# Optimization experiments

Hardware: AMD Instinct MI355X
Metric: run time of the kernel (lower is better)

The kernel has to match this reference:

```python
import jax, jax.numpy as jnp
import numpy as np

N_WIRES = 5
TOTAL = 2 * N_WIRES          # query branch simulates 2*n_wires qubits
DIM = 1 << TOTAL             # 1024
ENC = 1 << N_WIRES           # 32 = token encoder output dim


def setup_inputs() -> dict:
    key = jax.random.key(0)
    ks = jax.random.split(key, 6)
    B, T, C = 4, 32, 512
    x = jax.random.normal(ks[0], (B, T, C), jnp.float32)
    W_tok = jax.random.normal(ks[1], (ENC, C), jnp.float32) * 0.05
    b_tok = jax.random.normal(ks[2], (ENC,), jnp.float32) * 0.05
    theta_rx0 = jax.random.normal(ks[3], (TOTAL,), jnp.float32)
    theta_ry0 = jax.random.normal(ks[4], (TOTAL,), jnp.float32)
    theta_ry1 = jax.random.normal(ks[5], (TOTAL,), jnp.float32)
    return {"x": x, "W_tok": W_tok, "b_tok": b_tok,
            "theta_rx0": theta_rx0, "theta_ry0": theta_ry0, "theta_ry1": theta_ry1}


def _rx_mat(t):
    c = jnp.cos(t / 2).astype(jnp.complex64)
    s = jnp.sin(t / 2).astype(jnp.complex64)
    return jnp.stack([jnp.stack([c, -1j * s]), jnp.stack([-1j * s, c])])


def _ry_mat(t):
    c = jnp.cos(t / 2).astype(jnp.complex64)
    s = jnp.sin(t / 2).astype(jnp.complex64)
    return jnp.stack([jnp.stack([c, -s]), jnp.stack([s, c])])


def _apply_1q(state, U, w):
    # state: (bsz, 2, 2, ..., 2); wire w lives on axis 1+w (wire 0 = MSB)
    s = jnp.tensordot(state, U, axes=((1 + w,), (1,)))  # gate axis moves to last
    return jnp.moveaxis(s, -1, 1 + w)


def _apply_cnot(state, c, t):
    s = jnp.moveaxis(state, (1 + c, 1 + t), (-2, -1))
    s = s.at[..., 1, :].set(s[..., 1, ::-1])  # flip target where control == 1
    return jnp.moveaxis(s, (-2, -1), (1 + c, 1 + t))


def reference(x, W_tok, b_tok, theta_rx0, theta_ry0, theta_ry1):
    B, T, C = x.shape
    # token encoding + L2 normalize  -> (B, T, 32)
    enc = x @ W_tok.T + b_tok
    enc = enc / jnp.linalg.norm(enc, axis=-1, keepdims=True)
    # all T*T pairwise outer products, flattened as a_idx*32 + b_idx  -> (B, T*T, 1024)
    pairs = jnp.einsum('bip,bjq->bijpq', enc, enc).reshape(B, T * T, DIM)
    pairs = pairs / jnp.linalg.norm(pairs, axis=-1, keepdims=True)
    state = pairs.astype(jnp.complex64).reshape((B * T * T,) + (2,) * TOTAL)
    # layer 1: RX then RY on every wire
    for j in range(TOTAL):
        state = _apply_1q(state, _rx_mat(theta_rx0[j]), j)
        state = _apply_1q(state, _ry_mat(theta_ry0[j]), j)
    # CNOT ring
    for j in range(TOTAL):
        state = _apply_cnot(state, j, (j + 1) % TOTAL)
    # layer 2: RY on every wire
    for j in range(TOTAL):
        state = _apply_1q(state, _ry_mat(theta_ry1[j]), j)
    return state.reshape(B, T * T, DIM)
```

## Files before the change

kernel.cpp:

```cpp
#include <hip/hip_runtime.h>
#include <hip/hip_bf16.h>


__device__ __forceinline__ float2 cmulf(float2 a, float2 b) {
    return make_float2(a.x * b.x - a.y * b.y, a.x * b.y + a.y * b.x);
}
__device__ __forceinline__ float2 caddf(float2 a, float2 b) {
    return make_float2(a.x + b.x, a.y + b.y);
}

__global__ __launch_bounds__(256) void enc_kernel(const float* __restrict__ x,
                                                  const float* __restrict__ W,
                                                  const float* __restrict__ bt,
                                                  float* __restrict__ enc) {
    int row = blockIdx.x;
    int tid = threadIdx.x;
    int col = tid & 31;
    int seg = tid >> 5;
    const float* xs = x + (size_t)row * 512 + seg * 64;
    const float* ws = W + (size_t)col * 512 + seg * 64;
    float p = 0.f;
#pragma unroll
    for (int k = 0; k < 64; ++k) p += xs[k] * ws[k];
    __shared__ float part[8][32];
    part[seg][col] = p;
    __syncthreads();
    if (tid < 32) {
        float sum = bt[col];
#pragma unroll
        for (int g = 0; g < 8; ++g) sum += part[g][col];
        float sq = sum * sum;
#pragma unroll
        for (int off = 1; off < 32; off <<= 1) sq += __shfl_xor(sq, off, 64);
        enc[row * 32 + col] = sum * (1.0f / sqrtf(sq));
    }
}

__global__ __launch_bounds__(256) void build_F(const float* __restrict__ rx0,
                                               const float* __restrict__ ry0,
                                               const float* __restrict__ ry1,
                                               float2* __restrict__ F) {
    int tid = threadIdx.x;
    int side = tid >> 7;
    int s = (tid >> 6) & 1;
    int t = (tid >> 5) & 1;
    int k = tid & 31;

    float2 v[32];
#pragma unroll
    for (int m = 0; m < 32; ++m) v[m] = make_float2(m == k ? 1.f : 0.f, 0.f);

    int wbase = side * 5;
#pragma unroll
    for (int l = 0; l < 5; ++l) {
        float tx = rx0[wbase + l] * 0.5f, ty = ry0[wbase + l] * 0.5f;
        float cx = cosf(tx), sx = sinf(tx), cy = cosf(ty), sy = sinf(ty);
        float2 g00 = make_float2(cy * cx,  sy * sx);
        float2 g01 = make_float2(-sy * cx, -cy * sx);
        float2 g10 = make_float2(sy * cx,  -cy * sx);
        float2 g11 = make_float2(cy * cx,  -sy * sx);
        int bit = 1 << (4 - l);
#pragma unroll
        for (int m = 0; m < 32; ++m) {
            if (m & bit) continue;
            float2 a = v[m], b = v[m | bit];
            v[m]       = caddf(cmulf(g00, a), cmulf(g01, b));
            v[m | bit] = caddf(cmulf(g10, a), cmulf(g11, b));
        }
    }

    if (side == 0) {
#pragma unroll
        for (int l = 0; l < 4; ++l) {
            int cb = 1 << (4 - l), tb = 1 << (3 - l);
#pragma unroll
            for (int m = 0; m < 32; ++m) {
                if ((m & cb) && !(m & tb)) {
                    float2 tmp = v[m]; v[m] = v[m | tb]; v[m | tb] = tmp;
                }
            }
        }
#pragma unroll
        for (int m = 0; m < 32; ++m)
            if ((m & 1) != s) v[m] = make_float2(0.f, 0.f);
        if (t) {
#pragma unroll
            for (int m = 0; m < 16; ++m) {
                float2 tmp = v[m]; v[m] = v[m | 16]; v[m | 16] = tmp;
            }
        }
    } else {
        if (s) {
#pragma unroll
            for (int m = 0; m < 16; ++m) {
                float2 tmp = v[m]; v[m] = v[m | 16]; v[m | 16] = tmp;
            }
        }
#pragma unroll
        for (int l = 0; l < 4; ++l) {
            int cb = 1 << (4 - l), tb = 1 << (3 - l);
#pragma unroll
            for (int m = 0; m < 32; ++m) {
                if ((m & cb) && !(m & tb)) {
                    float2 tmp = v[m]; v[m] = v[m | tb]; v[m | tb] = tmp;
                }
            }
        }
#pragma unroll
        for (int m = 0; m < 32; ++m)
            if ((m & 1) != t) v[m] = make_float2(0.f, 0.f);
    }

#pragma unroll
    for (int l = 0; l < 5; ++l) {
        float ty = ry1[wbase + l] * 0.5f;
        float cy = cosf(ty), sy = sinf(ty);
        int bit = 1 << (4 - l);
#pragma unroll
        for (int m = 0; m < 32; ++m) {
            if (m & bit) continue;
            float2 a = v[m], b = v[m | bit];
            v[m]       = make_float2(cy * a.x - sy * b.x, cy * a.y - sy * b.y);
            v[m | bit] = make_float2(sy * a.x + cy * b.x, sy * a.y + cy * b.y);
        }
    }

    float2* dst = F + (size_t)(side * 4 + s * 2 + t) * 32 * 32;
#pragma unroll
    for (int p = 0; p < 32; ++p) dst[p * 32 + k] = v[p];
}

__global__ __launch_bounds__(256) void matvec_uv(const float2* __restrict__ F,
                                                 const float* __restrict__ enc,
                                                 float2* __restrict__ U,
                                                 float2* __restrict__ V) {
    int row = blockIdx.x;
    int tid = threadIdx.x;
    int side = tid >> 7;
    int st = (tid >> 5) & 3;
    int p = tid & 31;
    __shared__ float e[32];
    if (tid < 32) e[tid] = enc[row * 32 + tid];
    __syncthreads();
    const float2* Fr = F + ((size_t)(side * 4 + st) * 32 + p) * 32;
    float2 acc = make_float2(0.f, 0.f);
#pragma unroll
    for (int k = 0; k < 32; ++k) {
        float ev = e[k];
        acc.x += Fr[k].x * ev;
        acc.y += Fr[k].y * ev;
    }
    float2* dst = (side == 0) ? U : V;
    dst[(size_t)row * 128 + st * 32 + p] = acc;
}

__global__ __launch_bounds__(256) void outer_kernel(const float2* __restrict__ U,
                                                    const float2* __restrict__ V,
                                                    float* __restrict__ out,
                                                    int complex_out) {
    int bx = blockIdx.x;
    int b = blockIdx.y;
    int i = bx >> 5, j = bx & 31;
    int tid = threadIdx.x;
    __shared__ float2 su[128];
    __shared__ float2 sv[128];
    if (tid < 128) su[tid] = U[(size_t)(b * 32 + i) * 128 + tid];
    else           sv[tid - 128] = V[(size_t)(b * 32 + j) * 128 + (tid - 128)];
    __syncthreads();

    int d0 = tid << 2;
    int p = d0 >> 5;
    int q0 = d0 & 31;
    float2 up0 = su[p], up1 = su[32 + p], up2 = su[64 + p], up3 = su[96 + p];

    float2 acc[4];
#pragma unroll
    for (int e = 0; e < 4; ++e) {
        int q = q0 + e;
        float2 v0 = sv[q], v1 = sv[32 + q], v2 = sv[64 + q], v3 = sv[96 + q];
        float2 a;
        a.x = up0.x * v0.x - up0.y * v0.y + up1.x * v1.x - up1.y * v1.y
            + up2.x * v2.x - up2.y * v2.y + up3.x * v3.x - up3.y * v3.y;
        a.y = up0.x * v0.y + up0.y * v0.x + up1.x * v1.y + up1.y * v1.x
            + up2.x * v2.y + up2.y * v2.x + up3.x * v3.y + up3.y * v3.x;
        acc[e] = a;
    }

    size_t pair = (size_t)b * 1024 + bx;
    if (complex_out) {
        float4* o = (float4*)(out + (pair * 1024 + d0) * 2);
        o[0] = make_float4(acc[0].x, acc[0].y, acc[1].x, acc[1].y);
        o[1] = make_float4(acc[2].x, acc[2].y, acc[3].x, acc[3].y);
    } else {
        float4* o = (float4*)(out + pair * 1024 + d0);
        o[0] = make_float4(acc[0].x, acc[1].x, acc[2].x, acc[3].x);
    }
}

extern "C" void kernel_launch(void* const* d_in, const int* in_sizes, int n_in,
                              void* d_out, int out_size, void* d_ws, size_t ws_size,
                              hipStream_t stream) {
    const float* x   = (const float*)d_in[0];
    const float* W   = (const float*)d_in[1];
    const float* bt  = (const float*)d_in[2];
    const float* rx0 = (const float*)d_in[3];
    const float* ry0 = (const float*)d_in[4];
    const float* ry1 = (const float*)d_in[5];

    float2* F = (float2*)d_ws;
    float2* U = F + 8192;
    float2* V = U + 16384;
    float*  enc = (float*)(V + 16384);

    enc_kernel<<<128, 256, 0, stream>>>(x, W, bt, enc);
    build_F<<<1, 256, 0, stream>>>(rx0, ry0, ry1, F);
    matvec_uv<<<128, 256, 0, stream>>>(F, enc, U, V);

    int complex_out = (out_size > 4 * 1024 * 1024) ? 1 : 0;
    dim3 grid(1024, 4);
    outer_kernel<<<grid, 256, 0, stream>>>(U, V, (float*)d_out, complex_out);
}
```

Baseline: 87.95 us.

## Fuse encoder, circuit matrix build and matvec into one wave-shuffle prep kernel

Replaces three kernels (token encoder, single-block build_F that materialised 8 32x32 factor matrices, and matvec) with one kernel. Each block applies the gates directly to its encoded vector, one amplitude per lane, and exchanges partner amplitudes with cross-lane xor shuffles. This removes two launches, the serial single-block matrix build, and the global round-trip of F and enc. The cost is that every block now recomputes the trig and gate sequence itself, which is cheap. The output-bound outer kernel is unchanged, so it still dominates the runtime.

Result: faster. 79.62 us (-9.5%).

```diff
diff --git a/kernel.cpp b/kernel.cpp
--- a/kernel.cpp
+++ b/kernel.cpp
@@ -8,150 +8,97 @@
 __device__ __forceinline__ float2 caddf(float2 a, float2 b) {
     return make_float2(a.x + b.x, a.y + b.y);
 }
+__device__ __forceinline__ float2 shflx(float2 v, int mask) {
+    return make_float2(__shfl_xor(v.x, mask, 64), __shfl_xor(v.y, mask, 64));
+}
 
-__global__ __launch_bounds__(256) void enc_kernel(const float* __restrict__ x,
-                                                  const float* __restrict__ W,
-                                                  const float* __restrict__ bt,
-                                                  float* __restrict__ enc) {
+__global__ __launch_bounds__(256) void prep_kernel(const float* __restrict__ x,
+                                                   const float* __restrict__ W,
+                                                   const float* __restrict__ bt,
+                                                   const float* __restrict__ rx0,
+                                                   const float* __restrict__ ry0,
+                                                   const float* __restrict__ ry1,
+                                                   float2* __restrict__ U,
+                                                   float2* __restrict__ V) {
     int row = blockIdx.x;
     int tid = threadIdx.x;
     int col = tid & 31;
     int seg = tid >> 5;
     const float* xs = x + (size_t)row * 512 + seg * 64;
     const float* ws = W + (size_t)col * 512 + seg * 64;
-    float p = 0.f;
+    float part_acc = 0.f;
 #pragma unroll
-    for (int k = 0; k < 64; ++k) p += xs[k] * ws[k];
+    for (int k = 0; k < 64; ++k) part_acc += xs[k] * ws[k];
     __shared__ float part[8][32];
-    part[seg][col] = p;
+    __shared__ float e[32];
+    part[seg][col] = part_acc;
     __syncthreads();
     if (tid < 32) {
-        float sum = bt[col];
+        float sum = bt[tid];
 #pragma unroll
-        for (int g = 0; g < 8; ++g) sum += part[g][col];
+        for (int g = 0; g < 8; ++g) sum += part[g][tid];
         float sq = sum * sum;
 #pragma unroll
         for (int off = 1; off < 32; off <<= 1) sq += __shfl_xor(sq, off, 64);
-        enc[row * 32 + col] = sum * (1.0f / sqrtf(sq));
+        e[tid] = sum * (1.0f / sqrtf(sq));
     }
-}
+    __syncthreads();
 
-__global__ __launch_bounds__(256) void build_F(const float* __restrict__ rx0,
-                                               const float* __restrict__ ry0,
-                                               const float* __restrict__ ry1,
-                                               float2* __restrict__ F) {
-    int tid = threadIdx.x;
     int side = tid >> 7;
     int s = (tid >> 6) & 1;
     int t = (tid >> 5) & 1;
-    int k = tid & 31;
+    int p = tid & 31;
+    int wb = side * 5;
 
-    float2 v[32];
-#pragma unroll
-    for (int m = 0; m < 32; ++m) v[m] = make_float2(m == k ? 1.f : 0.f, 0.f);
+    float2 c = make_float2(e[p], 0.f);
 
-    int wbase = side * 5;
 #pragma unroll
     for (int l = 0; l < 5; ++l) {
-        float tx = rx0[wbase + l] * 0.5f, ty = ry0[wbase + l] * 0.5f;
+        float tx = rx0[wb + l] * 0.5f, ty = ry0[wb + l] * 0.5f;
         float cx = cosf(tx), sx = sinf(tx), cy = cosf(ty), sy = sinf(ty);
+        int bit = 1 << (4 - l);
+        float2 pr = shflx(c, bit);
         float2 g00 = make_float2(cy * cx,  sy * sx);
         float2 g01 = make_float2(-sy * cx, -cy * sx);
         float2 g10 = make_float2(sy * cx,  -cy * sx);
         float2 g11 = make_float2(cy * cx,  -sy * sx);
-        int bit = 1 << (4 - l);
-#pragma unroll
-        for (int m = 0; m < 32; ++m) {
-            if (m & bit) continue;
-            float2 a = v[m], b = v[m | bit];
-            v[m]       = caddf(cmulf(g00, a), cmulf(g01, b));
-            v[m | bit] = caddf(cmulf(g10, a), cmulf(g11, b));
-        }
+        c = ((p & bit) == 0) ? caddf(cmulf(g00, c), cmulf(g01, pr))
+                             : caddf(cmulf(g10, pr), cmulf(g11, c));
     }
 
     if (side == 0) {
 #pragma unroll
         for (int l = 0; l < 4; ++l) {
             int cb = 1 << (4 - l), tb = 1 << (3 - l);
-#pragma unroll
-            for (int m = 0; m < 32; ++m) {
-                if ((m & cb) && !(m & tb)) {
-                    float2 tmp = v[m]; v[m] = v[m | tb]; v[m | tb] = tmp;
-                }
-            }
+            float2 pr = shflx(c, tb);
+            if (p & cb) c = pr;
         }
-#pragma unroll
-        for (int m = 0; m < 32; ++m)
-            if ((m & 1) != s) v[m] = make_float2(0.f, 0.f);
-        if (t) {
-#pragma unroll
-            for (int m = 0; m < 16; ++m) {
-                float2 tmp = v[m]; v[m] = v[m | 16]; v[m | 16] = tmp;
-            }
-        }
+        if ((p & 1) != s) c = make_float2(0.f, 0.f);
+        { float2 pr = shflx(c, 16); if (t) c = pr; }
     } else {
-        if (s) {
-#pragma unroll
-            for (int m = 0; m < 16; ++m) {
-                float2 tmp = v[m]; v[m] = v[m | 16]; v[m | 16] = tmp;
-            }
-        }
+        { float2 pr = shflx(c, 16); if (s) c = pr; }
 #pragma unroll
         for (int l = 0; l < 4; ++l) {
             int cb = 1 << (4 - l), tb = 1 << (3 - l);
-#pragma unroll
-            for (int m = 0; m < 32; ++m) {
-                if ((m & cb) && !(m & tb)) {
-                    float2 tmp = v[m]; v[m] = v[m | tb]; v[m | tb] = tmp;
-                }
-            }
+            float2 pr = shflx(c, tb);
+            if (p & cb) c = pr;
         }
-#pragma unroll
-        for (int m = 0; m < 32; ++m)
-            if ((m & 1) != t) v[m] = make_float2(0.f, 0.f);
+        if ((p & 1) != t) c = make_float2(0.f, 0.f);
     }
 
 #pragma unroll
     for (int l = 0; l < 5; ++l) {
-        float ty = ry1[wbase + l] * 0.5f;
+        float ty = ry1[wb + l] * 0.5f;
         float cy = cosf(ty), sy = sinf(ty);
         int bit = 1 << (4 - l);
-#pragma unroll
-        for (int m = 0; m < 32; ++m) {
-            if (m & bit) continue;
-            float2 a = v[m], b = v[m | bit];
-            v[m]       = make_float2(cy * a.x - sy * b.x, cy * a.y - sy * b.y);
-            v[m | bit] = make_float2(sy * a.x + cy * b.x, sy * a.y + cy * b.y);
-        }
+        float2 pr = shflx(c, bit);
+        c = ((p & bit) == 0)
+              ? make_float2(cy * c.x - sy * pr.x, cy * c.y - sy * pr.y)
+              : make_float2(sy * pr.x + cy * c.x, sy * pr.y + cy * c.y);
     }
 
-    float2* dst = F + (size_t)(side * 4 + s * 2 + t) * 32 * 32;
-#pragma unroll
-    for (int p = 0; p < 32; ++p) dst[p * 32 + k] = v[p];
-}
-
-__global__ __launch_bounds__(256) void matvec_uv(const float2* __restrict__ F,
-                                                 const float* __restrict__ enc,
-                                                 float2* __restrict__ U,
-                                                 float2* __restrict__ V) {
-    int row = blockIdx.x;
-    int tid = threadIdx.x;
-    int side = tid >> 7;
-    int st = (tid >> 5) & 3;
-    int p = tid & 31;
-    __shared__ float e[32];
-    if (tid < 32) e[tid] = enc[row * 32 + tid];
-    __syncthreads();
-    const float2* Fr = F + ((size_t)(side * 4 + st) * 32 + p) * 32;
-    float2 acc = make_float2(0.f, 0.f);
-#pragma unroll
-    for (int k = 0; k < 32; ++k) {
-        float ev = e[k];
-        acc.x += Fr[k].x * ev;
-        acc.y += Fr[k].y * ev;
-    }
     float2* dst = (side == 0) ? U : V;
-    dst[(size_t)row * 128 + st * 32 + p] = acc;
+    dst[(size_t)row * 128 + (s * 2 + t) * 32 + p] = c;
 }
 
 __global__ __launch_bounds__(256) void outer_kernel(const float2* __restrict__ U,
@@ -207,14 +154,10 @@
     const float* ry0 = (const float*)d_in[4];
     const float* ry1 = (const float*)d_in[5];
 
-    float2* F = (float2*)d_ws;
-    float2* U = F + 8192;
+    float2* U = (float2*)d_ws;
     float2* V = U + 16384;
-    float*  enc = (float*)(V + 16384);
 
-    enc_kernel<<<128, 256, 0, stream>>>(x, W, bt, enc);
-    build_F<<<1, 256, 0, stream>>>(rx0, ry0, ry1, F);
-    matvec_uv<<<128, 256, 0, stream>>>(F, enc, U, V);
+    prep_kernel<<<128, 256, 0, stream>>>(x, W, bt, rx0, ry0, ry1, U, V);
 
     int complex_out = (out_size > 4 * 1024 * 1024) ? 1 : 0;
     dim3 grid(1024, 4);
```
